# Performance work log

Hardware: AMD Instinct MI355X
Metric: run time of the kernel (lower is better)

The kernel has to match this reference:

```python
import jax, jax.numpy as jnp
import numpy as np

B_, L, D = 4, 2048, 1024          # batch, seq_len, d_model
E = 2 * D                         # d_inner (expand=2)
N = 8                             # d_state
K = 4                             # d_conv
R = D // 16                       # dt_rank = 64
EPS = 1e-5


def silu(x):
    return x * jax.nn.sigmoid(x)


def setup_inputs() -> dict:
    key = jax.random.key(0)
    ks = jax.random.split(key, 8)
    s = 0.02
    inp = jax.random.normal(ks[0], (B_, L, D), jnp.float32)
    in_proj_w = jax.random.normal(ks[1], (2 * E, D), jnp.float32) * s
    conv_w = jax.random.normal(ks[2], (E, 1, K), jnp.float32) * s  # depthwise, OIW
    conv_b = jnp.zeros((E,), jnp.float32)
    x_proj_w = jax.random.normal(ks[3], (R + 2 * N, E), jnp.float32) * s
    dt_proj_w = jax.random.normal(ks[4], (E, R), jnp.float32) * s
    # bias so softplus(dt) gives realistic small timesteps
    dt_proj_b = jax.random.uniform(ks[5], (E,), jnp.float32, minval=-4.0, maxval=-2.0)
    # S4D-real init: A = -[1..N] per channel
    A_log = jnp.log(jnp.broadcast_to(jnp.arange(1, N + 1, dtype=jnp.float32), (E, N)))
    D_param = jnp.ones((E,), jnp.float32)
    out_proj_w = jax.random.normal(ks[6], (D, E), jnp.float32) * s
    rms_w = jnp.ones((D,), jnp.float32)
    return dict(inp=inp, in_proj_w=in_proj_w, conv_w=conv_w, conv_b=conv_b,
                x_proj_w=x_proj_w, dt_proj_w=dt_proj_w, dt_proj_b=dt_proj_b,
                A_log=A_log, D_param=D_param, out_proj_w=out_proj_w, rms_w=rms_w)


def reference(inp, in_proj_w, conv_w, conv_b, x_proj_w, dt_proj_w, dt_proj_b,
              A_log, D_param, out_proj_w, rms_w):
    b, l, d = inp.shape
    # input projection -> x (ssm branch) and z (gate branch), each (b, l, E)
    xz = inp @ in_proj_w.T
    x, z = jnp.split(xz, 2, axis=-1)
    # depthwise causal conv1d along time
    xt = x.transpose(0, 2, 1)                                   # (b, E, l)
    xc = jax.lax.conv_general_dilated(xt, conv_w, (1,), [(K - 1, 0)],
                                      feature_group_count=E)
    x = silu((xc + conv_b[None, :, None]).transpose(0, 2, 1))   # (b, l, E)
    # data-dependent SSM params
    dbc = x @ x_proj_w.T                                        # (b, l, R+2N)
    dt, Bm, Cm = jnp.split(dbc, [R, R + N], axis=-1)
    delta = jax.nn.softplus(dt @ dt_proj_w.T + dt_proj_b)       # (b, l, E)
    A = -jnp.exp(A_log)                                         # (E, N)

    def step(h, t):
        d_t, B_t, C_t, u_t = t                                  # (b,E),(b,N),(b,N),(b,E)
        dA = jnp.exp(d_t[..., None] * A)                        # (b, E, N)
        h = h * dA + (d_t * u_t)[..., None] * B_t[:, None, :]
        y = jnp.einsum('ben,bn->be', h, C_t)
        return h, y

    xs = (delta.transpose(1, 0, 2), Bm.transpose(1, 0, 2),
          Cm.transpose(1, 0, 2), x.transpose(1, 0, 2))
    h0 = jnp.zeros((b, E, N), inp.dtype)
    _, ys = jax.lax.scan(step, h0, xs)                          # ys: (l, b, E)
    y = ys.transpose(1, 0, 2) + x * D_param                     # skip term u*D
    y = y * silu(z)                                             # gating
    out = y @ out_proj_w.T                                      # (b, l, D)
    # RMSNorm
    out = out * jax.lax.rsqrt(jnp.mean(out * out, axis=-1, keepdims=True) + EPS) * rms_w
    # dropout p=0 -> identity
    return out
```

## Files before the change

kernel.cpp:

```cpp
#include <hip/hip_runtime.h>

#define LL 2048
#define EE 2048
#define DD 1024
#define NC 64
#define CH 32

typedef short bf16x8 __attribute__((ext_vector_type(8)));
typedef float f32x4 __attribute__((ext_vector_type(4)));

__device__ inline float bf2f(unsigned short u) {
    union { unsigned u; float f; } v; v.u = ((unsigned)u) << 16; return v.f;
}
__device__ inline unsigned short f2bf(float f) {
    union { float f; unsigned u; } v; v.f = f;
    unsigned r = v.u + 0x7fff + ((v.u >> 16) & 1);
    return (unsigned short)(r >> 16);
}

__device__ inline void gload_lds16(const void* g, void* lds) {
    __builtin_amdgcn_global_load_lds(
        (const __attribute__((address_space(1))) unsigned int*)g,
        (__attribute__((address_space(3))) unsigned int*)lds, 16, 0, 0);
}

template<int MODE, int BN>
__global__ __launch_bounds__(512, 2)
void gemm8p(const unsigned short* __restrict__ A,
            const unsigned short* __restrict__ Bw,
            void* __restrict__ Cout,
            const float* __restrict__ bias,
            int M, int N, int K)
{
    constexpr int NREP = BN / 64;
    constexpr int RB   = BN / 128;
    constexpr int LH   = 2 + RB;
    constexpr int NSTRIP = BN / 4;

    extern __shared__ short lds[];
    short* Asm = lds;
    short* Bsm = lds + 2 * 2 * 256 * 32;

    const int tid = threadIdx.x;
    const int w = tid >> 6, lane = tid & 63;
    const int wm = w >> 2, wn = w & 3;

    const int gx = N / BN;
    const int nwg = gx * (M / 256);
    int lin = blockIdx.y * gx + blockIdx.x;
    int swz = ((nwg & 7) == 0) ? ((lin & 7) * (nwg >> 3) + (lin >> 3)) : lin;
    const long m0 = (long)(swz / gx) * 256;
    const long n0 = (long)(swz % gx) * BN;

    const int g = (tid & 3) ^ ((tid >> 3) & 3);
    const int arow = tid >> 2;
    const unsigned short* Ag = A + (m0 + arow) * (long)K + g * 8;
    const unsigned short* Bg = Bw + (n0 + arow) * (long)K + g * 8;
    const int ldsrow = w * 16;

    auto stageA = [&](int buf, int kh, int j, int kt) {
        gload_lds16(Ag + (long)j * 128 * K + kt * 64 + kh * 32,
                    Asm + ((buf * 2 + kh) * 256 + j * 128 + ldsrow) * 32);
    };
    auto stageB = [&](int buf, int kh, int j, int kt) {
        gload_lds16(Bg + (long)j * 128 * K + kt * 64 + kh * 32,
                    Bsm + ((buf * 2 + kh) * BN + j * 128 + ldsrow) * 32);
    };

    f32x4 acc[8][NREP] = {};

    stageA(0, 0, 0, 0); stageA(0, 0, 1, 0);
#pragma unroll
    for (int j = 0; j < RB; ++j) stageB(0, 0, j, 0);
    stageA(0, 1, 0, 0); stageA(0, 1, 1, 0);
#pragma unroll
    for (int j = 0; j < RB; ++j) stageB(0, 1, j, 0);

    const int NT = K / 64;
    const int rr = lane & 15;
    const int sl = ((lane >> 4) ^ ((rr >> 1) & 3)) * 8;

    for (int t = 0; t < NT; ++t) {
        const int cur = t & 1, nxt = cur ^ 1;
        const bool more = (t + 1 < NT);

        asm volatile("s_waitcnt vmcnt(%0)" :: "i"(LH) : "memory");
        __builtin_amdgcn_s_barrier();

        const short* Ac0 = Asm + (cur * 2 + 0) * 256 * 32;
        const short* Bc0 = Bsm + (cur * 2 + 0) * BN * 32;
        if (more) { stageA(nxt, 0, 0, t + 1); stageA(nxt, 0, 1, t + 1); }
        bf16x8 a[4], b[NREP];
#pragma unroll
        for (int m = 0; m < 4; ++m)
            a[m] = *(const bf16x8*)&Ac0[(wm * 128 + m * 16 + rr) * 32 + sl];
#pragma unroll
        for (int n = 0; n < NREP; ++n)
            b[n] = *(const bf16x8*)&Bc0[(wn * NSTRIP + n * 16 + rr) * 32 + sl];
        __builtin_amdgcn_s_setprio(1);
#pragma unroll
        for (int m = 0; m < 4; ++m)
#pragma unroll
            for (int n = 0; n < NREP; ++n)
                acc[m][n] = __builtin_amdgcn_mfma_f32_16x16x32_bf16(a[m], b[n], acc[m][n], 0, 0, 0);
        __builtin_amdgcn_s_setprio(0);
        if (more) {
#pragma unroll
            for (int j = 0; j < RB; ++j) stageB(nxt, 0, j, t + 1);
        }
#pragma unroll
        for (int m = 0; m < 4; ++m)
            a[m] = *(const bf16x8*)&Ac0[(wm * 128 + 64 + m * 16 + rr) * 32 + sl];
        __builtin_amdgcn_s_setprio(1);
#pragma unroll
        for (int m = 0; m < 4; ++m)
#pragma unroll
            for (int n = 0; n < NREP; ++n)
                acc[4 + m][n] = __builtin_amdgcn_mfma_f32_16x16x32_bf16(a[m], b[n], acc[4 + m][n], 0, 0, 0);
        __builtin_amdgcn_s_setprio(0);

        if (more) { asm volatile("s_waitcnt vmcnt(%0)" :: "i"(LH) : "memory"); }
        else      { asm volatile("s_waitcnt vmcnt(0)" ::: "memory"); }
        __builtin_amdgcn_s_barrier();

        const short* Ac1 = Asm + (cur * 2 + 1) * 256 * 32;
        const short* Bc1 = Bsm + (cur * 2 + 1) * BN * 32;
        if (more) { stageA(nxt, 1, 0, t + 1); stageA(nxt, 1, 1, t + 1); }
#pragma unroll
        for (int m = 0; m < 4; ++m)
            a[m] = *(const bf16x8*)&Ac1[(wm * 128 + m * 16 + rr) * 32 + sl];
#pragma unroll
        for (int n = 0; n < NREP; ++n)
            b[n] = *(const bf16x8*)&Bc1[(wn * NSTRIP + n * 16 + rr) * 32 + sl];
        __builtin_amdgcn_s_setprio(1);
#pragma unroll
        for (int m = 0; m < 4; ++m)
#pragma unroll
            for (int n = 0; n < NREP; ++n)
                acc[m][n] = __builtin_amdgcn_mfma_f32_16x16x32_bf16(a[m], b[n], acc[m][n], 0, 0, 0);
        __builtin_amdgcn_s_setprio(0);
        if (more) {
#pragma unroll
            for (int j = 0; j < RB; ++j) stageB(nxt, 1, j, t + 1);
        }
#pragma unroll
        for (int m = 0; m < 4; ++m)
            a[m] = *(const bf16x8*)&Ac1[(wm * 128 + 64 + m * 16 + rr) * 32 + sl];
        __builtin_amdgcn_s_setprio(1);
#pragma unroll
        for (int m = 0; m < 4; ++m)
#pragma unroll
            for (int n = 0; n < NREP; ++n)
                acc[4 + m][n] = __builtin_amdgcn_mfma_f32_16x16x32_bf16(a[m], b[n], acc[4 + m][n], 0, 0, 0);
        __builtin_amdgcn_s_setprio(0);
    }

#pragma unroll
    for (int m = 0; m < 8; ++m) {
#pragma unroll
        for (int n = 0; n < NREP; ++n) {
#pragma unroll
            for (int r = 0; r < 4; ++r) {
                long row = m0 + wm * 128 + m * 16 + (lane >> 4) * 4 + r;
                long col = n0 + wn * NSTRIP + n * 16 + (lane & 15);
                float v = acc[m][n][r];
                if (MODE == 0) {
                    ((float*)Cout)[row * N + col] = v;
                } else if (MODE == 1) {
                    ((unsigned short*)Cout)[row * N + col] = f2bf(v);
                } else {
                    v += bias[col];
                    float sp = (v > 20.f) ? v : log1pf(__expf(v));
                    ((unsigned short*)Cout)[row * N + col] = f2bf(sp);
                }
            }
        }
    }
}

__global__ __launch_bounds__(256)
void gemm_xp(const unsigned short* __restrict__ A,
             const unsigned short* __restrict__ Bw,
             float* __restrict__ Cout)
{
    __shared__ short As[128 * 32];
    __shared__ short Bs[128 * 32];
    const int tid = threadIdx.x;
    const int wave = tid >> 6, lane = tid & 63;
    const int wm = wave >> 1, wn = wave & 1;
    const long m0 = (long)blockIdx.x * 128;
    const int kz = blockIdx.y;
    float* out = Cout + (long)kz * 8192 * 128;

    f32x4 acc[4][4] = {};

    const int srow = lane >> 2;
    const int g = (lane & 3) ^ ((srow >> 1) & 3);
    const int c0 = wave, c1 = wave + 4;

    for (int k0 = kz * 256; k0 < kz * 256 + 256; k0 += 32) {
        gload_lds16(A + (m0 + c0 * 16 + srow) * 2048L + k0 + g * 8, &As[c0 * 16 * 32]);
        gload_lds16(A + (m0 + c1 * 16 + srow) * 2048L + k0 + g * 8, &As[c1 * 16 * 32]);
        gload_lds16(Bw + (c0 * 16 + srow) * 2048L + k0 + g * 8, &Bs[c0 * 16 * 32]);
        gload_lds16(Bw + (c1 * 16 + srow) * 2048L + k0 + g * 8, &Bs[c1 * 16 * 32]);
        __syncthreads();

        const int rr = lane & 15;
        const int sl = ((lane >> 4) ^ ((rr >> 1) & 3)) * 8;
        bf16x8 af[4], bfr[4];
#pragma unroll
        for (int m = 0; m < 4; ++m)
            af[m] = *(const bf16x8*)&As[(wm * 64 + m * 16 + rr) * 32 + sl];
#pragma unroll
        for (int n = 0; n < 4; ++n)
            bfr[n] = *(const bf16x8*)&Bs[(wn * 64 + n * 16 + rr) * 32 + sl];
#pragma unroll
        for (int m = 0; m < 4; ++m)
#pragma unroll
            for (int n = 0; n < 4; ++n)
                acc[m][n] = __builtin_amdgcn_mfma_f32_16x16x32_bf16(af[m], bfr[n], acc[m][n], 0, 0, 0);
        __syncthreads();
    }

#pragma unroll
    for (int m = 0; m < 4; ++m)
#pragma unroll
        for (int n = 0; n < 4; ++n)
#pragma unroll
            for (int r = 0; r < 4; ++r) {
                long row = m0 + wm * 64 + m * 16 + (lane >> 4) * 4 + r;
                long col = wn * 64 + n * 16 + (lane & 15);
                out[row * 128 + col] = acc[m][n][r];
            }
}

__global__ void reduce_dbc(const float* __restrict__ part,
                           float* __restrict__ dbc,
                           unsigned short* __restrict__ dt)
{
    const long i = (long)blockIdx.x * 256 + threadIdx.x;
    float s = 0.f;
#pragma unroll
    for (int k = 0; k < 8; ++k) s += part[i + (long)k * 1048576];
    dbc[i] = s;
    const int c = (int)(i & 127);
    if (c < 64) dt[(i >> 7) * 64 + c] = f2bf(s);
}

__device__ inline void cvt4(const float* __restrict__ in, unsigned short* __restrict__ out, long i) {
    float4 v = ((const float4*)in)[i];
    unsigned lo = (unsigned)f2bf(v.x) | ((unsigned)f2bf(v.y) << 16);
    unsigned hi = (unsigned)f2bf(v.z) | ((unsigned)f2bf(v.w) << 16);
    ((uint2*)out)[i] = make_uint2(lo, hi);
}

__global__ void cvt_all(const float* __restrict__ inp, const float* __restrict__ w_in,
                        const float* __restrict__ w_xp, const float* __restrict__ w_dt,
                        const float* __restrict__ w_out,
                        unsigned short* __restrict__ o_inp, unsigned short* __restrict__ o_win,
                        unsigned short* __restrict__ o_wxp, unsigned short* __restrict__ o_wdt,
                        unsigned short* __restrict__ o_wout)
{
    const long t = (long)blockIdx.x * 256 + threadIdx.x;
    const long gs = (long)gridDim.x * 256;
    for (long i = t; i < 8388608 / 4; i += gs) cvt4(inp, o_inp, i);
    for (long i = t; i < 4194304 / 4; i += gs) cvt4(w_in, o_win, i);
    for (long i = t; i < 2097152 / 4; i += gs) cvt4(w_out, o_wout, i);
    for (long i = t; i < 131072 / 4; i += gs) cvt4(w_dt, o_wdt, i);
    for (long i = t; i < 262144 / 4; i += gs) {
        const int r = (int)(i >> 9);
        if (r < 80) cvt4(w_xp, o_wxp, i);
        else ((uint2*)o_wxp)[i] = make_uint2(0u, 0u);
    }
}

__global__ void conv_silu_k(const unsigned short* __restrict__ xz,
                            const float* __restrict__ cw,
                            const float* __restrict__ cb,
                            unsigned short* __restrict__ xc)
{
    const int ep = blockIdx.y * 256 + threadIdx.x;
    const int e0 = ep * 2, e1 = e0 + 1;
    const int b = blockIdx.z;
    const int l0 = blockIdx.x * 32;
    const float wa0 = cw[e0 * 4], wa1 = cw[e0 * 4 + 1], wa2 = cw[e0 * 4 + 2], wa3 = cw[e0 * 4 + 3];
    const float wb0 = cw[e1 * 4], wb1 = cw[e1 * 4 + 1], wb2 = cw[e1 * 4 + 2], wb3 = cw[e1 * 4 + 3];
    const float ba = cb[e0], bb = cb[e1];
    const unsigned* xrow = (const unsigned*)(xz + (long)b * LL * 4096) + ep;
    unsigned* orow = (unsigned*)(xc + (long)b * LL * 2048) + ep;

    float a3 = 0.f, a2 = 0.f, a1 = 0.f, b3 = 0.f, b2 = 0.f, b1 = 0.f;
    if (l0 >= 3) { unsigned u = xrow[(long)(l0 - 3) * 2048]; a3 = bf2f(u & 0xffff); b3 = bf2f(u >> 16); }
    if (l0 >= 2) { unsigned u = xrow[(long)(l0 - 2) * 2048]; a2 = bf2f(u & 0xffff); b2 = bf2f(u >> 16); }
    if (l0 >= 1) { unsigned u = xrow[(long)(l0 - 1) * 2048]; a1 = bf2f(u & 0xffff); b1 = bf2f(u >> 16); }
    for (int l = l0; l < l0 + 32; ++l) {
        unsigned u = xrow[(long)l * 2048];
        float xa = bf2f(u & 0xffff), xb = bf2f(u >> 16);
        float va = ba + wa0 * a3 + wa1 * a2 + wa2 * a1 + wa3 * xa;
        float vb = bb + wb0 * b3 + wb1 * b2 + wb2 * b1 + wb3 * xb;
        float sa = va / (1.f + __expf(-va));
        float sb = vb / (1.f + __expf(-vb));
        orow[(long)l * 1024] = (unsigned)f2bf(sa) | ((unsigned)f2bf(sb) << 16);
        a3 = a2; a2 = a1; a1 = xa;
        b3 = b2; b2 = b1; b1 = xb;
    }
}

__global__ __launch_bounds__(256)
void scan_local(const unsigned short* __restrict__ delta,
                const unsigned short* __restrict__ xconv,
                const float* __restrict__ dbc,
                const float* __restrict__ A_log,
                float* __restrict__ hend, float* __restrict__ Ssum)
{
    const int e = blockIdx.x * 256 + threadIdx.x;
    const int c = blockIdx.y, b = blockIdx.z;
    const int l0 = c * CH;
    float An[8];
#pragma unroll
    for (int n = 0; n < 8; ++n) An[n] = -__expf(A_log[e * 8 + n]);
    float h[8] = {};
    float S = 0.f;
    const unsigned short* drow = delta + ((long)b * LL + l0) * EE + e;
    const unsigned short* urow = xconv + ((long)b * LL + l0) * EE + e;
    const float* bc = dbc + ((long)b * LL + l0) * 128;
    for (int l = 0; l < CH; ++l) {
        float d = bf2f(drow[(long)l * EE]);
        float u = bf2f(urow[(long)l * EE]);
        float du = d * u;
        S += d;
#pragma unroll
        for (int n = 0; n < 8; ++n)
            h[n] = h[n] * __expf(d * An[n]) + du * bc[l * 128 + 64 + n];
    }
    const long o = ((long)b * NC + c) * EE + e;
#pragma unroll
    for (int n = 0; n < 8; ++n) hend[o * 8 + n] = h[n];
    Ssum[o] = S;
}

__global__ __launch_bounds__(256)
void scan_combine(const float* __restrict__ hend, const float* __restrict__ Ssum,
                  const float* __restrict__ A_log, float* __restrict__ hin)
{
    const int t = blockIdx.x * 256 + threadIdx.x;
    const int b = t >> 11, e = t & 2047;
    float An[8];
#pragma unroll
    for (int n = 0; n < 8; ++n) An[n] = -__expf(A_log[e * 8 + n]);
    float h[8] = {};
    for (int c = 0; c < NC; ++c) {
        const long o = ((long)b * NC + c) * EE + e;
#pragma unroll
        for (int n = 0; n < 8; ++n) hin[o * 8 + n] = h[n];
        float S = Ssum[o];
#pragma unroll
        for (int n = 0; n < 8; ++n)
            h[n] = h[n] * __expf(An[n] * S) + hend[o * 8 + n];
    }
}

__global__ __launch_bounds__(256)
void scan_final(const unsigned short* __restrict__ delta,
                const unsigned short* __restrict__ xconv,
                const float* __restrict__ dbc,
                const unsigned short* __restrict__ xz,
                const float* __restrict__ A_log,
                const float* __restrict__ Dparam,
                const float* __restrict__ hin,
                unsigned short* __restrict__ yg)
{
    const int e = blockIdx.x * 256 + threadIdx.x;
    const int c = blockIdx.y, b = blockIdx.z;
    const int l0 = c * CH;
    float An[8];
#pragma unroll
    for (int n = 0; n < 8; ++n) An[n] = -__expf(A_log[e * 8 + n]);
    const float Dp = Dparam[e];
    float h[8];
    const long o = ((long)b * NC + c) * EE + e;
#pragma unroll
    for (int n = 0; n < 8; ++n) h[n] = hin[o * 8 + n];
    const unsigned short* drow = delta + ((long)b * LL + l0) * EE + e;
    const unsigned short* urow = xconv + ((long)b * LL + l0) * EE + e;
    const unsigned short* zrow = xz + ((long)b * LL + l0) * 4096 + 2048 + e;
    const float* bc = dbc + ((long)b * LL + l0) * 128;
    unsigned short* yrow = yg + ((long)b * LL + l0) * EE + e;
    for (int l = 0; l < CH; ++l) {
        float d = bf2f(drow[(long)l * EE]);
        float u = bf2f(urow[(long)l * EE]);
        float du = d * u;
        float y = 0.f;
#pragma unroll
        for (int n = 0; n < 8; ++n) {
            h[n] = h[n] * __expf(d * An[n]) + du * bc[l * 128 + 64 + n];
            y += h[n] * bc[l * 128 + 72 + n];
        }
        y += u * Dp;
        float z = bf2f(zrow[(long)l * 4096]);
        float g = z / (1.f + __expf(-z));
        yrow[(long)l * EE] = f2bf(y * g);
    }
}

__global__ __launch_bounds__(256)
void rmsnorm_k(const unsigned short* __restrict__ in, const float* __restrict__ w,
               float* __restrict__ out)
{
    const int row = blockIdx.x;
    uint2 v2 = *(const uint2*)(in + (long)row * 1024 + threadIdx.x * 4);
    float x0 = bf2f(v2.x & 0xffff), x1 = bf2f(v2.x >> 16);
    float x2 = bf2f(v2.y & 0xffff), x3 = bf2f(v2.y >> 16);
    float ss = x0 * x0 + x1 * x1 + x2 * x2 + x3 * x3;
#pragma unroll
    for (int m = 32; m >= 1; m >>= 1) ss += __shfl_xor(ss, m, 64);
    __shared__ float wsum[4];
    const int wave = threadIdx.x >> 6;
    if ((threadIdx.x & 63) == 0) wsum[wave] = ss;
    __syncthreads();
    float tot = wsum[0] + wsum[1] + wsum[2] + wsum[3];
    float sc = rsqrtf(tot * (1.f / 1024.f) + 1e-5f);
    float4 wv = ((const float4*)w)[threadIdx.x];
    float4 o;
    o.x = x0 * sc * wv.x; o.y = x1 * sc * wv.y;
    o.z = x2 * sc * wv.z; o.w = x3 * sc * wv.w;
    ((float4*)(out + (long)row * 1024))[threadIdx.x] = o;
}

extern "C" void kernel_launch(void* const* d_in, const int* in_sizes, int n_in,
                              void* d_out, int out_size, void* d_ws, size_t ws_size,
                              hipStream_t stream)
{
    const float* inp   = (const float*)d_in[0];
    const float* w_in  = (const float*)d_in[1];
    const float* convw = (const float*)d_in[2];
    const float* convb = (const float*)d_in[3];
    const float* w_xp  = (const float*)d_in[4];
    const float* w_dt  = (const float*)d_in[5];
    const float* b_dt  = (const float*)d_in[6];
    const float* A_log = (const float*)d_in[7];
    const float* Dp    = (const float*)d_in[8];
    const float* w_out = (const float*)d_in[9];
    const float* rmsw  = (const float*)d_in[10];

    char* ws = (char*)d_ws;
    const size_t MB = 1024 * 1024;
    unsigned short* inp_bf   = (unsigned short*)(ws + 0);
    unsigned short* win_bf   = (unsigned short*)(ws + 16 * MB);
    unsigned short* xz_bf    = (unsigned short*)(ws + 24 * MB);
    unsigned short* xconv_bf = (unsigned short*)(ws + 88 * MB);
    unsigned short* wxp_bf   = (unsigned short*)(ws + 120 * MB);
    float*          dbc      = (float*)(ws + 121 * MB);
    unsigned short* dt_bf    = (unsigned short*)(ws + 125 * MB);
    unsigned short* wdt_bf   = (unsigned short*)(ws + 126 * MB);
    unsigned short* delta_bf = (unsigned short*)(ws + 127 * MB);
    unsigned short* yg_bf    = (unsigned short*)(ws + 191 * MB);
    unsigned short* wout_bf  = (unsigned short*)(ws + 223 * MB);
    float*          dbc_part = (float*)(ws + 159 * MB);
    float*          hend     = (float*)(ws + 159 * MB);
    float*          hin      = (float*)(ws + 175 * MB);
    float*          Ssum     = (float*)(ws + 0);
    unsigned short* out_pre  = (unsigned short*)(ws + 0);

    hipFuncSetAttribute((const void*)gemm8p<1, 256>, hipFuncAttributeMaxDynamicSharedMemorySize, 131072);
    hipFuncSetAttribute((const void*)gemm8p<2, 128>, hipFuncAttributeMaxDynamicSharedMemorySize, 98304);
    hipFuncSetAttribute((const void*)gemm8p<1, 128>, hipFuncAttributeMaxDynamicSharedMemorySize, 98304);

    cvt_all<<<2048, 256, 0, stream>>>(inp, w_in, w_xp, w_dt, w_out,
                                      inp_bf, win_bf, wxp_bf, wdt_bf, wout_bf);

    gemm8p<1, 256><<<dim3(16, 32), 512, 131072, stream>>>(inp_bf, win_bf, xz_bf, nullptr, 8192, 4096, 1024);
    conv_silu_k<<<dim3(64, 4, 4), 256, 0, stream>>>(xz_bf, convw, convb, xconv_bf);
    gemm_xp<<<dim3(64, 8), 256, 0, stream>>>(xconv_bf, wxp_bf, dbc_part);
    reduce_dbc<<<4096, 256, 0, stream>>>(dbc_part, dbc, dt_bf);
    gemm8p<2, 128><<<dim3(16, 32), 512, 98304, stream>>>(dt_bf, wdt_bf, delta_bf, b_dt, 8192, 2048, 64);
    scan_local<<<dim3(8, NC, 4), 256, 0, stream>>>(delta_bf, xconv_bf, dbc, A_log, hend, Ssum);
    scan_combine<<<32, 256, 0, stream>>>(hend, Ssum, A_log, hin);
    scan_final<<<dim3(8, NC, 4), 256, 0, stream>>>(delta_bf, xconv_bf, dbc, xz_bf, A_log, Dp, hin, yg_bf);
    gemm8p<1, 128><<<dim3(8, 32), 512, 98304, stream>>>(yg_bf, wout_bf, out_pre, nullptr, 8192, 1024, 2048);
    rmsnorm_k<<<8192, 256, 0, stream>>>(out_pre, rmsw, (float*)d_out);
}
```

Baseline: 334.5 us.

## Restructure GEMM main loop into four barrier-phased stages; vectorize scans over channel pairs

The GEMM main loop is restructured into a four-phase schedule. Each phase reads LDS fragments, issues the next global-to-LDS loads, then runs an explicit barrier, lgkmcnt wait and sched_barrier before its MFMA burst, with an extra barrier after each burst. The aim is to keep waves in lockstep and interleave the memory traffic with compute more deterministically, at the cost of more barriers per K-step. Separately, the scan_local and scan_final kernels now handle two channels per thread with 32-bit packed bf16 loads and stores, halving the grid and reusing B/C loads across both channels.

```diff
diff --git a/kernel.cpp b/kernel.cpp
--- a/kernel.cpp
+++ b/kernel.cpp
@@ -26,7 +26,7 @@
 
 template<int MODE, int BN>
 __global__ __launch_bounds__(512, 2)
-void gemm8p(const unsigned short* __restrict__ A,
+void gemm4p(const unsigned short* __restrict__ A,
             const unsigned short* __restrict__ Bw,
             void* __restrict__ Cout,
             const float* __restrict__ bias,
@@ -75,6 +75,8 @@
     stageA(0, 1, 0, 0); stageA(0, 1, 1, 0);
 #pragma unroll
     for (int j = 0; j < RB; ++j) stageB(0, 1, j, 0);
+    asm volatile("s_waitcnt vmcnt(%0)" :: "i"(LH) : "memory");
+    __builtin_amdgcn_s_barrier();
 
     const int NT = K / 64;
     const int rr = lane & 15;
@@ -83,20 +85,22 @@
     for (int t = 0; t < NT; ++t) {
         const int cur = t & 1, nxt = cur ^ 1;
         const bool more = (t + 1 < NT);
-
-        asm volatile("s_waitcnt vmcnt(%0)" :: "i"(LH) : "memory");
-        __builtin_amdgcn_s_barrier();
-
         const short* Ac0 = Asm + (cur * 2 + 0) * 256 * 32;
         const short* Bc0 = Bsm + (cur * 2 + 0) * BN * 32;
-        if (more) { stageA(nxt, 0, 0, t + 1); stageA(nxt, 0, 1, t + 1); }
+        const short* Ac1 = Asm + (cur * 2 + 1) * 256 * 32;
+        const short* Bc1 = Bsm + (cur * 2 + 1) * BN * 32;
         bf16x8 a[4], b[NREP];
-#pragma unroll
-        for (int m = 0; m < 4; ++m)
-            a[m] = *(const bf16x8*)&Ac0[(wm * 128 + m * 16 + rr) * 32 + sl];
+
 #pragma unroll
         for (int n = 0; n < NREP; ++n)
             b[n] = *(const bf16x8*)&Bc0[(wn * NSTRIP + n * 16 + rr) * 32 + sl];
+#pragma unroll
+        for (int m = 0; m < 4; ++m)
+            a[m] = *(const bf16x8*)&Ac0[(wm * 128 + m * 16 + rr) * 32 + sl];
+        if (more) { stageA(nxt, 0, 0, t + 1); stageA(nxt, 0, 1, t + 1); }
+        __builtin_amdgcn_s_barrier();
+        asm volatile("s_waitcnt lgkmcnt(0)" ::: "memory");
+        __builtin_amdgcn_sched_barrier(0);
         __builtin_amdgcn_s_setprio(1);
 #pragma unroll
         for (int m = 0; m < 4; ++m)
@@ -104,13 +108,21 @@
             for (int n = 0; n < NREP; ++n)
                 acc[m][n] = __builtin_amdgcn_mfma_f32_16x16x32_bf16(a[m], b[n], acc[m][n], 0, 0, 0);
         __builtin_amdgcn_s_setprio(0);
+        __builtin_amdgcn_s_barrier();
+
+#pragma unroll
+        for (int m = 0; m < 4; ++m)
+            a[m] = *(const bf16x8*)&Ac0[(wm * 128 + 64 + m * 16 + rr) * 32 + sl];
         if (more) {
 #pragma unroll
             for (int j = 0; j < RB; ++j) stageB(nxt, 0, j, t + 1);
+            asm volatile("s_waitcnt vmcnt(%0)" :: "i"(LH) : "memory");
+        } else {
+            asm volatile("s_waitcnt vmcnt(0)" ::: "memory");
         }
-#pragma unroll
-        for (int m = 0; m < 4; ++m)
-            a[m] = *(const bf16x8*)&Ac0[(wm * 128 + 64 + m * 16 + rr) * 32 + sl];
+        __builtin_amdgcn_s_barrier();
+        asm volatile("s_waitcnt lgkmcnt(0)" ::: "memory");
+        __builtin_amdgcn_sched_barrier(0);
         __builtin_amdgcn_s_setprio(1);
 #pragma unroll
         for (int m = 0; m < 4; ++m)
@@ -118,20 +130,18 @@
             for (int n = 0; n < NREP; ++n)
                 acc[4 + m][n] = __builtin_amdgcn_mfma_f32_16x16x32_bf16(a[m], b[n], acc[4 + m][n], 0, 0, 0);
         __builtin_amdgcn_s_setprio(0);
-
-        if (more) { asm volatile("s_waitcnt vmcnt(%0)" :: "i"(LH) : "memory"); }
-        else      { asm volatile("s_waitcnt vmcnt(0)" ::: "memory"); }
-        __builtin_amdgcn_s_barrier();
-
-        const short* Ac1 = Asm + (cur * 2 + 1) * 256 * 32;
-        const short* Bc1 = Bsm + (cur * 2 + 1) * BN * 32;
-        if (more) { stageA(nxt, 1, 0, t + 1); stageA(nxt, 1, 1, t + 1); }
-#pragma unroll
-        for (int m = 0; m < 4; ++m)
-            a[m] = *(const bf16x8*)&Ac1[(wm * 128 + m * 16 + rr) * 32 + sl];
+        __builtin_amdgcn_s_barrier();
+
 #pragma unroll
         for (int n = 0; n < NREP; ++n)
             b[n] = *(const bf16x8*)&Bc1[(wn * NSTRIP + n * 16 + rr) * 32 + sl];
+#pragma unroll
+        for (int m = 0; m < 4; ++m)
+            a[m] = *(const bf16x8*)&Ac1[(wm * 128 + m * 16 + rr) * 32 + sl];
+        if (more) { stageA(nxt, 1, 0, t + 1); stageA(nxt, 1, 1, t + 1); }
+        __builtin_amdgcn_s_barrier();
+        asm volatile("s_waitcnt lgkmcnt(0)" ::: "memory");
+        __builtin_amdgcn_sched_barrier(0);
         __builtin_amdgcn_s_setprio(1);
 #pragma unroll
         for (int m = 0; m < 4; ++m)
@@ -139,13 +149,19 @@
             for (int n = 0; n < NREP; ++n)
                 acc[m][n] = __builtin_amdgcn_mfma_f32_16x16x32_bf16(a[m], b[n], acc[m][n], 0, 0, 0);
         __builtin_amdgcn_s_setprio(0);
+        __builtin_amdgcn_s_barrier();
+
+#pragma unroll
+        for (int m = 0; m < 4; ++m)
+            a[m] = *(const bf16x8*)&Ac1[(wm * 128 + 64 + m * 16 + rr) * 32 + sl];
         if (more) {
 #pragma unroll
             for (int j = 0; j < RB; ++j) stageB(nxt, 1, j, t + 1);
+            asm volatile("s_waitcnt vmcnt(%0)" :: "i"(LH) : "memory");
         }
-#pragma unroll
-        for (int m = 0; m < 4; ++m)
-            a[m] = *(const bf16x8*)&Ac1[(wm * 128 + 64 + m * 16 + rr) * 32 + sl];
+        __builtin_amdgcn_s_barrier();
+        asm volatile("s_waitcnt lgkmcnt(0)" ::: "memory");
+        __builtin_amdgcn_sched_barrier(0);
         __builtin_amdgcn_s_setprio(1);
 #pragma unroll
         for (int m = 0; m < 4; ++m)
@@ -153,6 +169,7 @@
             for (int n = 0; n < NREP; ++n)
                 acc[4 + m][n] = __builtin_amdgcn_mfma_f32_16x16x32_bf16(a[m], b[n], acc[4 + m][n], 0, 0, 0);
         __builtin_amdgcn_s_setprio(0);
+        __builtin_amdgcn_s_barrier();
     }
 
 #pragma unroll
@@ -313,30 +330,36 @@
                 const float* __restrict__ A_log,
                 float* __restrict__ hend, float* __restrict__ Ssum)
 {
-    const int e = blockIdx.x * 256 + threadIdx.x;
+    const int ep = blockIdx.x * 256 + threadIdx.x;
+    const int e0 = ep * 2;
     const int c = blockIdx.y, b = blockIdx.z;
     const int l0 = c * CH;
-    float An[8];
-#pragma unroll
-    for (int n = 0; n < 8; ++n) An[n] = -__expf(A_log[e * 8 + n]);
-    float h[8] = {};
-    float S = 0.f;
-    const unsigned short* drow = delta + ((long)b * LL + l0) * EE + e;
-    const unsigned short* urow = xconv + ((long)b * LL + l0) * EE + e;
+    float An[16];
+#pragma unroll
+    for (int n = 0; n < 16; ++n) An[n] = -__expf(A_log[e0 * 8 + n]);
+    float h[16] = {};
+    float S0 = 0.f, S1 = 0.f;
+    const unsigned* drow = (const unsigned*)(delta + ((long)b * LL + l0) * EE) + ep;
+    const unsigned* urow = (const unsigned*)(xconv + ((long)b * LL + l0) * EE) + ep;
     const float* bc = dbc + ((long)b * LL + l0) * 128;
     for (int l = 0; l < CH; ++l) {
-        float d = bf2f(drow[(long)l * EE]);
-        float u = bf2f(urow[(long)l * EE]);
-        float du = d * u;
-        S += d;
-#pragma unroll
-        for (int n = 0; n < 8; ++n)
-            h[n] = h[n] * __expf(d * An[n]) + du * bc[l * 128 + 64 + n];
-    }
-    const long o = ((long)b * NC + c) * EE + e;
-#pragma unroll
-    for (int n = 0; n < 8; ++n) hend[o * 8 + n] = h[n];
-    Ssum[o] = S;
+        unsigned dv = drow[(long)l * 1024];
+        unsigned uv = urow[(long)l * 1024];
+        float d0 = bf2f(dv & 0xffff), d1 = bf2f(dv >> 16);
+        float u0 = bf2f(uv & 0xffff), u1 = bf2f(uv >> 16);
+        float du0 = d0 * u0, du1 = d1 * u1;
+        S0 += d0; S1 += d1;
+#pragma unroll
+        for (int n = 0; n < 8; ++n) {
+            float bn = bc[l * 128 + 64 + n];
+            h[n]     = h[n]     * __expf(d0 * An[n])     + du0 * bn;
+            h[8 + n] = h[8 + n] * __expf(d1 * An[8 + n]) + du1 * bn;
+        }
+    }
+    const long o = ((long)b * NC + c) * EE + e0;
+#pragma unroll
+    for (int n = 0; n < 8; ++n) { hend[o * 8 + n] = h[n]; hend[(o + 1) * 8 + n] = h[8 + n]; }
+    Ssum[o] = S0; Ssum[o + 1] = S1;
 }
 
 __global__ __launch_bounds__(256)
@@ -370,36 +393,45 @@
                 const float* __restrict__ hin,
                 unsigned short* __restrict__ yg)
 {
-    const int e = blockIdx.x * 256 + threadIdx.x;
+    const int ep = blockIdx.x * 256 + threadIdx.x;
+    const int e0 = ep * 2;
     const int c = blockIdx.y, b = blockIdx.z;
     const int l0 = c * CH;
-    float An[8];
-#pragma unroll
-    for (int n = 0; n < 8; ++n) An[n] = -__expf(A_log[e * 8 + n]);
-    const float Dp = Dparam[e];
-    float h[8];
-    const long o = ((long)b * NC + c) * EE + e;
-#pragma unroll
-    for (int n = 0; n < 8; ++n) h[n] = hin[o * 8 + n];
-    const unsigned short* drow = delta + ((long)b * LL + l0) * EE + e;
-    const unsigned short* urow = xconv + ((long)b * LL + l0) * EE + e;
-    const unsigned short* zrow = xz + ((long)b * LL + l0) * 4096 + 2048 + e;
+    float An[16];
+#pragma unroll
+    for (int n = 0; n < 16; ++n) An[n] = -__expf(A_log[e0 * 8 + n]);
+    const float Dp0 = Dparam[e0], Dp1 = Dparam[e0 + 1];
+    float h[16];
+    const long o = ((long)b * NC + c) * EE + e0;
+#pragma unroll
+    for (int n = 0; n < 8; ++n) { h[n] = hin[o * 8 + n]; h[8 + n] = hin[(o + 1) * 8 + n]; }
+    const unsigned* drow = (const unsigned*)(delta + ((long)b * LL + l0) * EE) + ep;
+    const unsigned* urow = (const unsigned*)(xconv + ((long)b * LL + l0) * EE) + ep;
+    const unsigned* zrow = (const unsigned*)(xz + ((long)b * LL + l0) * 4096 + 2048) + ep;
     const float* bc = dbc + ((long)b * LL + l0) * 128;
-    unsigned short* yrow = yg + ((long)b * LL + l0) * EE + e;
+    unsigned* yrow = (unsigned*)(yg + ((long)b * LL + l0) * EE) + ep;
     for (int l = 0; l < CH; ++l) {
-        float d = bf2f(drow[(long)l * EE]);
-        float u = bf2f(urow[(long)l * EE]);
-        float du = d * u;
-        float y = 0.f;
+        unsigned dv = drow[(long)l * 1024];
+        unsigned uv = urow[(long)l * 1024];
+        float d0 = bf2f(dv & 0xffff), d1 = bf2f(dv >> 16);
+        float u0 = bf2f(uv & 0xffff), u1 = bf2f(uv >> 16);
+        float du0 = d0 * u0, du1 = d1 * u1;
+        float y0 = 0.f, y1 = 0.f;
 #pragma unroll
         for (int n = 0; n < 8; ++n) {
-            h[n] = h[n] * __expf(d * An[n]) + du * bc[l * 128 + 64 + n];
-            y += h[n] * bc[l * 128 + 72 + n];
+            float bn = bc[l * 128 + 64 + n];
+            float cn = bc[l * 128 + 72 + n];
+            h[n]     = h[n]     * __expf(d0 * An[n])     + du0 * bn;
+            h[8 + n] = h[8 + n] * __expf(d1 * An[8 + n]) + du1 * bn;
+            y0 += h[n] * cn;
+            y1 += h[8 + n] * cn;
         }
-        y += u * Dp;
-        float z = bf2f(zrow[(long)l * 4096]);
-        float g = z / (1.f + __expf(-z));
-        yrow[(long)l * EE] = f2bf(y * g);
+        y0 += u0 * Dp0; y1 += u1 * Dp1;
+        unsigned zv = zrow[(long)l * 2048];
+        float z0 = bf2f(zv & 0xffff), z1 = bf2f(zv >> 16);
+        float g0 = z0 / (1.f + __expf(-z0));
+        float g1 = z1 / (1.f + __expf(-z1));
+        yrow[(long)l * 1024] = (unsigned)f2bf(y0 * g0) | ((unsigned)f2bf(y1 * g1) << 16);
     }
 }
 
@@ -462,21 +494,21 @@
     float*          Ssum     = (float*)(ws + 0);
     unsigned short* out_pre  = (unsigned short*)(ws + 0);
 
-    hipFuncSetAttribute((const void*)gemm8p<1, 256>, hipFuncAttributeMaxDynamicSharedMemorySize, 131072);
-    hipFuncSetAttribute((const void*)gemm8p<2, 128>, hipFuncAttributeMaxDynamicSharedMemorySize, 98304);
-    hipFuncSetAttribute((const void*)gemm8p<1, 128>, hipFuncAttributeMaxDynamicSharedMemorySize, 98304);
+    hipFuncSetAttribute((const void*)gemm4p<1, 256>, hipFuncAttributeMaxDynamicSharedMemorySize, 131072);
+    hipFuncSetAttribute((const void*)gemm4p<2, 128>, hipFuncAttributeMaxDynamicSharedMemorySize, 98304);
+    hipFuncSetAttribute((const void*)gemm4p<1, 128>, hipFuncAttributeMaxDynamicSharedMemorySize, 98304);
 
     cvt_all<<<2048, 256, 0, stream>>>(inp, w_in, w_xp, w_dt, w_out,
                                       inp_bf, win_bf, wxp_bf, wdt_bf, wout_bf);
 
-    gemm8p<1, 256><<<dim3(16, 32), 512, 131072, stream>>>(inp_bf, win_bf, xz_bf, nullptr, 8192, 4096, 1024);
+    gemm4p<1, 256><<<dim3(16, 32), 512, 131072, stream>>>(inp_bf, win_bf, xz_bf, nullptr, 8192, 4096, 1024);
     conv_silu_k<<<dim3(64, 4, 4), 256, 0, stream>>>(xz_bf, convw, convb, xconv_bf);
     gemm_xp<<<dim3(64, 8), 256, 0, stream>>>(xconv_bf, wxp_bf, dbc_part);
     reduce_dbc<<<4096, 256, 0, stream>>>(dbc_part, dbc, dt_bf);
-    gemm8p<2, 128><<<dim3(16, 32), 512, 98304, stream>>>(dt_bf, wdt_bf, delta_bf, b_dt, 8192, 2048, 64);
-    scan_local<<<dim3(8, NC, 4), 256, 0, stream>>>(delta_bf, xconv_bf, dbc, A_log, hend, Ssum);
+    gemm4p<2, 128><<<dim3(16, 32), 512, 98304, stream>>>(dt_bf, wdt_bf, delta_bf, b_dt, 8192, 2048, 64);
+    scan_local<<<dim3(4, NC, 4), 256, 0, stream>>>(delta_bf, xconv_bf, dbc, A_log, hend, Ssum);
     scan_combine<<<32, 256, 0, stream>>>(hend, Ssum, A_log, hin);
-    scan_final<<<dim3(8, NC, 4), 256, 0, stream>>>(delta_bf, xconv_bf, dbc, xz_bf, A_log, Dp, hin, yg_bf);
-    gemm8p<1, 128><<<dim3(8, 32), 512, 98304, stream>>>(yg_bf, wout_bf, out_pre, nullptr, 8192, 1024, 2048);
+    scan_final<<<dim3(4, NC, 4), 256, 0, stream>>>(delta_bf, xconv_bf, dbc, xz_bf, A_log, Dp, hin, yg_bf);
+    gemm4p<1, 128><<<dim3(8, 32), 512, 98304, stream>>>(yg_bf, wout_bf, out_pre, nullptr, 8192, 1024, 2048);
     rmsnorm_k<<<8192, 256, 0, stream>>>(out_pre, rmsw, (float*)d_out);
 }
```

Measured after the change: 339.0 us. About the same (+1.3%).
